# Performance work log

Measured on AMD Instinct MI355X. Metric: run time of the kernel, lower is better.

## Reference

```python
import jax, jax.numpy as jnp
import numpy as np
from jax import lax

B, CIN, H, W = 32, 256, 28, 28
COUT, KS, KEXP = 256, 3, 4
HIDDEN = int(CIN * 0.25)  # ratio hard-coded to 0.25 in the module


def setup_inputs() -> dict:
    key = jax.random.key(0)
    k1, k2, k3, k4 = jax.random.split(key, 4)
    x = jax.random.normal(k1, (B, CIN, H, W), dtype=jnp.float32)
    # SE (InvertedEx) params: fc1 (1x1 conv, no bias), fc2 (1x1 conv, bias)
    fc1_w = jax.random.normal(k2, (HIDDEN, CIN), dtype=jnp.float32) * np.float32(np.sqrt(2.0 / CIN))
    fc2_w = jax.random.normal(k3, (KEXP * COUT, HIDDEN), dtype=jnp.float32) * np.float32(np.sqrt(2.0 / HIDDEN))
    fc2_b = jnp.zeros((KEXP * COUT,), dtype=jnp.float32)
    # K expert conv kernels, he_std = sqrt(2) * (CIN*KS^2)^-0.5
    he_std = np.float32(np.sqrt(2.0) * (CIN * KS * KS) ** -0.5)
    weight = jax.random.normal(k4, (KEXP, COUT, CIN, KS, KS), dtype=jnp.float32) * he_std
    return {"x": x, "fc1_w": fc1_w, "fc2_w": fc2_w, "fc2_b": fc2_b, "weight": weight}


def reference(x, fc1_w, fc2_w, fc2_b, weight):
    # --- SE routing ---
    pooled = jnp.mean(x, axis=(2, 3))                        # [B, CIN]
    h = jax.nn.relu(pooled @ fc1_w.T)                        # [B, HIDDEN]
    y = (h @ fc2_w.T + fc2_b).reshape(B, KEXP, COUT)         # [B, K, COUT]
    prob = jax.nn.softmax(y / jnp.sqrt(jnp.float32(HIDDEN)), axis=1)  # softmax over K
    # --- aggregate per-sample kernels ---
    agg_w = jnp.einsum('bko,koihw->boihw', prob, weight)     # [B, COUT, CIN, KS, KS]
    # --- per-sample conv (batched implicit GEMM via vmap) ---
    def conv1(xi, wi):
        return lax.conv_general_dilated(
            xi[None], wi, window_strides=(1, 1), padding=((1, 1), (1, 1)),
            dimension_numbers=('NCHW', 'OIHW', 'NCHW'))[0]
    out = jax.vmap(conv1)(x, agg_w)                          # [B, COUT, H, W]
    return out
```

## Files before the change

### kernel.cpp

```cpp
#include <hip/hip_runtime.h>
#include <math.h>

#define B_    32
#define CIN_  256
#define HW_   784
#define H_    28
#define W_    28
#define COUT_ 256
#define KEXP_ 4
#define HID_  64

typedef short short8 __attribute__((ext_vector_type(8)));
typedef unsigned short ushort4v __attribute__((ext_vector_type(4)));
typedef float floatx16 __attribute__((ext_vector_type(16)));

__device__ __forceinline__ unsigned short f2bf(float f) {
    union { float f; unsigned int u; } v; v.f = f;
    unsigned int r = (v.u + 0x7FFFu + ((v.u >> 16) & 1u)) >> 16;
    return (unsigned short)r;
}

__global__ __launch_bounds__(256) void xpose_pool_kernel(const float* __restrict__ x,
                                                         unsigned short* __restrict__ x_t,
                                                         float* __restrict__ partial) {
    __shared__ float tile[32][33];
    int bid = blockIdx.x;
    int b   = bid / 200;
    int rem = bid - b * 200;
    int icg = rem / 25;
    int pxt = rem % 25;
    int ic0 = icg * 32;
    int px0 = pxt * 32;
    int t = threadIdx.x;
    int c = t & 31, rr = t >> 5;
    #pragma unroll
    for (int r = 0; r < 4; ++r) {
        int icr = rr + r * 8;
        int px = px0 + c;
        float v = (px < HW_) ? x[((size_t)(b * CIN_ + ic0 + icr)) * HW_ + px] : 0.f;
        tile[icr][c] = v;
    }
    __syncthreads();
    #pragma unroll
    for (int r = 0; r < 4; ++r) {
        int pxr = rr + r * 8;
        int px = px0 + pxr;
        if (px < HW_)
            x_t[((size_t)b * HW_ + px) * CIN_ + ic0 + c] = f2bf(tile[c][pxr]);
    }
    if (t < 32) {
        float s = 0.f;
        #pragma unroll
        for (int cc = 0; cc < 32; ++cc) s += tile[t][cc];
        partial[((size_t)b * 25 + pxt) * CIN_ + ic0 + t] = s * (1.0f / HW_);
    }
}

__global__ __launch_bounds__(256) void pool_kernel(const float* __restrict__ x,
                                                   float* __restrict__ pooled) {
    int w = blockIdx.x * 4 + (threadIdx.x >> 6);
    int lane = threadIdx.x & 63;
    const float* p = x + (size_t)w * HW_;
    float s = 0.f;
    for (int i = lane; i < HW_; i += 64) s += p[i];
    for (int off = 32; off; off >>= 1) s += __shfl_down(s, off);
    if (lane == 0) pooled[w] = s * (1.0f / HW_);
}

__global__ __launch_bounds__(256) void se3_kernel(const float* __restrict__ partial,
                                                  const float* __restrict__ fc1_w,
                                                  const float* __restrict__ fc2_w,
                                                  const float* __restrict__ fc2_b,
                                                  float* __restrict__ prob) {
    __shared__ float pl[CIN_];
    __shared__ float h[HID_];
    __shared__ float wb[16640];
    int b = blockIdx.x, t = threadIdx.x;
    {
        float s = 0.f;
        for (int pt = 0; pt < 25; ++pt)
            s += partial[((size_t)b * 25 + pt) * CIN_ + t];
        pl[t] = s;
    }
    #pragma unroll
    for (int i = 0; i < 16; ++i) {
        int l = t + i * 256;
        float4 v = *(const float4*)(fc1_w + (size_t)l * 4);
        int r = l >> 6, cc = (l & 63) * 4;
        float* dst = &wb[r * 257 + cc];
        dst[0] = v.x; dst[1] = v.y; dst[2] = v.z; dst[3] = v.w;
    }
    __syncthreads();
    if (t < HID_) {
        float s = 0.f;
        const float* wr = &wb[t * 257];
        for (int c = 0; c < CIN_; ++c) s += pl[c] * wr[c];
        h[t] = fmaxf(s, 0.f);
    }
    float yk[KEXP_];
    for (int k = 0; k < KEXP_; ++k) {
        __syncthreads();
        #pragma unroll
        for (int i = 0; i < 16; ++i) {
            int l = t + i * 256;
            float4 v = *(const float4*)(fc2_w + (size_t)k * COUT_ * HID_ + (size_t)l * 4);
            int o = l >> 4, jj = (l & 15) * 4;
            float* dst = &wb[o * 65 + jj];
            dst[0] = v.x; dst[1] = v.y; dst[2] = v.z; dst[3] = v.w;
        }
        __syncthreads();
        float s = fc2_b[k * COUT_ + t];
        const float* wr = &wb[t * 65];
        #pragma unroll
        for (int j = 0; j < HID_; ++j) s += h[j] * wr[j];
        yk[k] = s * 0.125f;
    }
    float m = yk[0];
    for (int k = 1; k < KEXP_; ++k) m = fmaxf(m, yk[k]);
    float e[KEXP_], sum = 0.f;
    for (int k = 0; k < KEXP_; ++k) { e[k] = expf(yk[k] - m); sum += e[k]; }
    float inv = 1.0f / sum;
    for (int k = 0; k < KEXP_; ++k)
        prob[b * (KEXP_ * COUT_) + k * COUT_ + t] = e[k] * inv;
}

__global__ __launch_bounds__(256) void se2_kernel(const float* __restrict__ pooled,
                                                  const float* __restrict__ fc1_w,
                                                  const float* __restrict__ fc2_w,
                                                  const float* __restrict__ fc2_b,
                                                  float* __restrict__ prob) {
    __shared__ float pl[CIN_];
    __shared__ float h[HID_];
    __shared__ float wb[16640];
    int b = blockIdx.x, t = threadIdx.x;
    pl[t] = pooled[b * CIN_ + t];
    #pragma unroll
    for (int i = 0; i < 16; ++i) {
        int l = t + i * 256;
        float4 v = *(const float4*)(fc1_w + (size_t)l * 4);
        int r = l >> 6, cc = (l & 63) * 4;
        float* dst = &wb[r * 257 + cc];
        dst[0] = v.x; dst[1] = v.y; dst[2] = v.z; dst[3] = v.w;
    }
    __syncthreads();
    if (t < HID_) {
        float s = 0.f;
        const float* wr = &wb[t * 257];
        for (int c = 0; c < CIN_; ++c) s += pl[c] * wr[c];
        h[t] = fmaxf(s, 0.f);
    }
    float yk[KEXP_];
    for (int k = 0; k < KEXP_; ++k) {
        __syncthreads();
        #pragma unroll
        for (int i = 0; i < 16; ++i) {
            int l = t + i * 256;
            float4 v = *(const float4*)(fc2_w + (size_t)k * COUT_ * HID_ + (size_t)l * 4);
            int o = l >> 4, jj = (l & 15) * 4;
            float* dst = &wb[o * 65 + jj];
            dst[0] = v.x; dst[1] = v.y; dst[2] = v.z; dst[3] = v.w;
        }
        __syncthreads();
        float s = fc2_b[k * COUT_ + t];
        const float* wr = &wb[t * 65];
        #pragma unroll
        for (int j = 0; j < HID_; ++j) s += h[j] * wr[j];
        yk[k] = s * 0.125f;
    }
    float m = yk[0];
    for (int k = 1; k < KEXP_; ++k) m = fmaxf(m, yk[k]);
    float e[KEXP_], sum = 0.f;
    for (int k = 0; k < KEXP_; ++k) { e[k] = expf(yk[k] - m); sum += e[k]; }
    float inv = 1.0f / sum;
    for (int k = 0; k < KEXP_; ++k)
        prob[b * (KEXP_ * COUT_) + k * COUT_ + t] = e[k] * inv;
}

__global__ __launch_bounds__(256) void agg3_kernel(const float* __restrict__ weight,
                                                   const float* __restrict__ prob,
                                                   unsigned short* __restrict__ agg) {
    __shared__ float ws_w[KEXP_ * CIN_ * 9];
    __shared__ float pb[KEXP_][8];
    int bid = blockIdx.x;
    int oc = bid & 255;
    int b0 = (bid >> 8) * 8;
    int t = threadIdx.x;
    #pragma unroll
    for (int i = 0; i < 9; ++i) {
        int e4 = t + i * 256;
        int k = e4 / 576;
        int r4 = e4 - k * 576;
        float4 v = *(const float4*)(weight + (size_t)k * 589824 + (size_t)oc * 2304 + (size_t)r4 * 4);
        *(float4*)&ws_w[e4 * 4] = v;
    }
    if (t < KEXP_ * 8) {
        int k = t >> 3, bb = t & 7;
        pb[k][bb] = prob[(size_t)(b0 + bb) * (KEXP_ * COUT_) + k * COUT_ + oc];
    }
    __syncthreads();
    int icg = t & 63, blane = t >> 6;
    for (int rs = 0; rs < 9; ++rs) {
        float wv[4][4];
        #pragma unroll
        for (int q = 0; q < 4; ++q)
            #pragma unroll
            for (int k = 0; k < 4; ++k)
                wv[q][k] = ws_w[k * 2304 + (icg * 4 + q) * 9 + rs];
        #pragma unroll
        for (int bb = 0; bb < 2; ++bb) {
            int bidx = blane * 2 + bb;
            float p0 = pb[0][bidx], p1 = pb[1][bidx], p2 = pb[2][bidx], p3 = pb[3][bidx];
            ushort4v pack;
            #pragma unroll
            for (int q = 0; q < 4; ++q) {
                float s = p0 * wv[q][0] + p1 * wv[q][1] + p2 * wv[q][2] + p3 * wv[q][3];
                pack[q] = f2bf(s);
            }
            *(ushort4v*)(agg + ((((size_t)(b0 + bidx) * 9 + rs) * COUT_ + oc)) * CIN_ + icg * 4) = pack;
        }
    }
}

__global__ __launch_bounds__(256, 1) void conv_mfma3_kernel(const unsigned short* __restrict__ x_t,
                                                            const unsigned short* __restrict__ agg,
                                                            float* __restrict__ out) {
    __shared__ __align__(16) short Xs[2][9 * 35 * 72];

    int gid = blockIdx.x;
    int b      = gid & 31;
    int oc0    = ((gid >> 5) & 1) * 128;
    int rowblk = gid >> 6;
    int py0 = rowblk * 7;

    int t = threadIdx.x;
    int lane = t & 63, w = t >> 6;
    int ml = lane & 31, kh = lane >> 5;

    floatx16 acc[7];
    #pragma unroll
    for (int j = 0; j < 7; ++j)
        #pragma unroll
        for (int r = 0; r < 16; ++r) acc[j][r] = 0.f;

    const unsigned short* xtb = x_t + (size_t)b * HW_ * CIN_;
    const unsigned short* aln = agg + (((size_t)b * 9 * COUT_) + oc0 + w * 32 + ml) * CIN_ + kh * 8;

    {
        #pragma unroll
        for (int i = 0; i < 10; ++i) {
            int l = t + i * 256;
            if (l < 2520) {
                int pos = l >> 3, g = l & 7;
                int row = pos / 35, col = pos - row * 35;
                int gy = py0 - 1 + row, gx = col - 1;
                short8 v = (short8)0;
                if ((unsigned)gy < 28u && (unsigned)gx < 28u)
                    v = *(const short8*)(xtb + ((size_t)(gy * W_ + gx)) * CIN_ + g * 8);
                *(short8*)&Xs[0][pos * 72 + g * 8] = v;
            }
        }
    }

    short8 Acur0, Acur1, Acur2, Anext0, Anext1, Anext2;
    Acur0 = *(const short8*)(aln + (size_t)(0 * 3 + 0) * (COUT_ * CIN_));
    Acur1 = *(const short8*)(aln + (size_t)(1 * 3 + 0) * (COUT_ * CIN_));
    Acur2 = *(const short8*)(aln + (size_t)(2 * 3 + 0) * (COUT_ * CIN_));
    int dxn = 1, kkn = 0, icn = 0;

    __syncthreads();

    for (int c = 0; c < 4; ++c) {
        int ic0 = c * 64;
        const short* xb = &Xs[c & 1][0];

        short8 Xl[10];
        if (c < 3) {
            #pragma unroll
            for (int i = 0; i < 10; ++i) {
                int l = t + i * 256;
                short8 v = (short8)0;
                if (l < 2520) {
                    int pos = l >> 3, g = l & 7;
                    int row = pos / 35, col = pos - row * 35;
                    int gy = py0 - 1 + row, gx = col - 1;
                    if ((unsigned)gy < 28u && (unsigned)gx < 28u)
                        v = *(const short8*)(xtb + ((size_t)(gy * W_ + gx)) * CIN_ + ic0 + 64 + g * 8);
                }
                Xl[i] = v;
            }
        }

        for (int kk = 0; kk < 4; ++kk) {
            for (int dx = 0; dx < 3; ++dx) {
                if (icn < 256) {
                    const unsigned short* ap = aln + icn + kkn * 16;
                    Anext0 = *(const short8*)(ap + (size_t)(0 * 3 + dxn) * (COUT_ * CIN_));
                    Anext1 = *(const short8*)(ap + (size_t)(1 * 3 + dxn) * (COUT_ * CIN_));
                    Anext2 = *(const short8*)(ap + (size_t)(2 * 3 + dxn) * (COUT_ * CIN_));
                    ++dxn;
                    if (dxn == 3) { dxn = 0; ++kkn; if (kkn == 4) { kkn = 0; icn += 64; } }
                }
                int va = (ml + dx) * 72 + kk * 16 + kh * 8;
                #pragma unroll
                for (int r = 0; r < 9; ++r) {
                    short8 Bf = *(const short8*)&xb[r * 2520 + va];
                    if (r <= 6)
                        acc[r]     = __builtin_amdgcn_mfma_f32_32x32x16_bf16(Acur0, Bf, acc[r], 0, 0, 0);
                    if (r >= 1 && r - 1 <= 6)
                        acc[r - 1] = __builtin_amdgcn_mfma_f32_32x32x16_bf16(Acur1, Bf, acc[r - 1], 0, 0, 0);
                    if (r >= 2)
                        acc[r - 2] = __builtin_amdgcn_mfma_f32_32x32x16_bf16(Acur2, Bf, acc[r - 2], 0, 0, 0);
                }
                Acur0 = Anext0; Acur1 = Anext1; Acur2 = Anext2;
            }
        }

        if (c < 3) {
            short* dstb = &Xs[(c & 1) ^ 1][0];
            #pragma unroll
            for (int i = 0; i < 10; ++i) {
                int l = t + i * 256;
                if (l < 2520) {
                    int pos = l >> 3, g = l & 7;
                    *(short8*)&dstb[pos * 72 + g * 8] = Xl[i];
                }
            }
        }
        __syncthreads();
    }

    if (ml < W_) {
        #pragma unroll
        for (int j = 0; j < 7; ++j) {
            float* op = out + ((size_t)(b * COUT_ + oc0 + w * 32)) * HW_ + (py0 + j) * W_ + ml;
            #pragma unroll
            for (int r = 0; r < 16; ++r) {
                int ocd = (r & 3) + 8 * (r >> 2) + 4 * kh;
                op[(size_t)ocd * HW_] = acc[j][r];
            }
        }
    }
}

__global__ __launch_bounds__(256) void conv_kernel(const float* __restrict__ x,
                                                   const float* __restrict__ weight,
                                                   const float* __restrict__ prob,
                                                   float* __restrict__ out) {
    __shared__ float xs[30 * 30];
    __shared__ float wagg[8][32][12];
    __shared__ float pl[KEXP_][8];

    int b  = blockIdx.x >> 5;
    int o0 = (blockIdx.x & 31) * 8;
    int t  = threadIdx.x;

    if (t < 32) {
        int k = t >> 3, oc = t & 7;
        pl[k][oc] = prob[b * (KEXP_ * COUT_) + k * COUT_ + o0 + oc];
    }
    int p0 = t;
    int pr[4], pc[4];
    bool pv[4];
    #pragma unroll
    for (int j = 0; j < 4; ++j) {
        int p = p0 + j * 256;
        pv[j] = p < HW_;
        pr[j] = p / W_;
        pc[j] = p % W_;
    }
    float acc[8][4];
    #pragma unroll
    for (int oc = 0; oc < 8; ++oc)
        #pragma unroll
        for (int j = 0; j < 4; ++j) acc[oc][j] = 0.f;

    int aoc = t >> 5, aii = t & 31;

    for (int ic0 = 0; ic0 < CIN_; ic0 += 32) {
        __syncthreads();
        {
            float w9[9];
            #pragma unroll
            for (int j = 0; j < 9; ++j) w9[j] = 0.f;
            int i = ic0 + aii;
            #pragma unroll
            for (int k = 0; k < KEXP_; ++k) {
                float pk = pl[k][aoc];
                const float* wp = weight + ((size_t)(k * COUT_ + o0 + aoc) * CIN_ + i) * 9;
                #pragma unroll
                for (int j = 0; j < 9; ++j) w9[j] += pk * wp[j];
            }
            #pragma unroll
            for (int j = 0; j < 9; ++j) wagg[aoc][aii][j] = w9[j];
        }
        for (int ii = 0; ii < 32; ++ii) {
            int i = ic0 + ii;
            __syncthreads();
            const float* xp = x + (size_t)(b * CIN_ + i) * HW_;
            for (int e = t; e < 900; e += 256) {
                int ry = e / 30, cx = e - ry * 30;
                int gy = ry - 1, gx = cx - 1;
                float v = 0.f;
                if ((unsigned)gy < 28u && (unsigned)gx < 28u) v = xp[gy * W_ + gx];
                xs[e] = v;
            }
            __syncthreads();
            float xv[4][9];
            #pragma unroll
            for (int j = 0; j < 4; ++j) {
                if (pv[j]) {
                    const float* xr = &xs[pr[j] * 30 + pc[j]];
                    xv[j][0] = xr[0];  xv[j][1] = xr[1];  xv[j][2] = xr[2];
                    xv[j][3] = xr[30]; xv[j][4] = xr[31]; xv[j][5] = xr[32];
                    xv[j][6] = xr[60]; xv[j][7] = xr[61]; xv[j][8] = xr[62];
                } else {
                    #pragma unroll
                    for (int q = 0; q < 9; ++q) xv[j][q] = 0.f;
                }
            }
            #pragma unroll
            for (int oc = 0; oc < 8; ++oc) {
                float4 wa = *(const float4*)&wagg[oc][ii][0];
                float4 wb2 = *(const float4*)&wagg[oc][ii][4];
                float  wc = wagg[oc][ii][8];
                #pragma unroll
                for (int j = 0; j < 4; ++j) {
                    acc[oc][j] += xv[j][0] * wa.x + xv[j][1] * wa.y + xv[j][2] * wa.z
                                + xv[j][3] * wa.w + xv[j][4] * wb2.x + xv[j][5] * wb2.y
                                + xv[j][6] * wb2.z + xv[j][7] * wb2.w + xv[j][8] * wc;
                }
            }
        }
    }
    #pragma unroll
    for (int oc = 0; oc < 8; ++oc) {
        float* op = out + (size_t)(b * COUT_ + o0 + oc) * HW_ + p0;
        #pragma unroll
        for (int j = 0; j < 4; ++j)
            if (pv[j]) op[j * 256] = acc[oc][j];
    }
}

extern "C" void kernel_launch(void* const* d_in, const int* in_sizes, int n_in,
                              void* d_out, int out_size, void* d_ws, size_t ws_size,
                              hipStream_t stream) {
    const float* x     = (const float*)d_in[0];
    const float* fc1_w = (const float*)d_in[1];
    const float* fc2_w = (const float*)d_in[2];
    const float* fc2_b = (const float*)d_in[3];
    const float* weight= (const float*)d_in[4];
    float* out = (float*)d_out;

    char* ws = (char*)d_ws;
    float* prob = (float*)(ws);
    unsigned short* x_t = (unsigned short*)(ws + 131072);
    unsigned short* agg = (unsigned short*)(ws + 12976128);
    float* partial = (float*)(ws + 12976128);
    const size_t WS_NEED = 12976128 + (size_t)B_ * 9 * COUT_ * CIN_ * 2;

    if (ws_size >= WS_NEED) {
        xpose_pool_kernel<<<B_ * 8 * 25, 256, 0, stream>>>(x, x_t, partial);
        se3_kernel<<<B_, 256, 0, stream>>>(partial, fc1_w, fc2_w, fc2_b, prob);
        agg3_kernel<<<4 * COUT_, 256, 0, stream>>>(weight, prob, agg);
        conv_mfma3_kernel<<<256, 256, 0, stream>>>(x_t, agg, out);
    } else {
        float* pooled = (float*)(ws + 131072);
        pool_kernel<<<(B_ * CIN_) / 4, 256, 0, stream>>>(x, pooled);
        se2_kernel<<<B_, 256, 0, stream>>>(pooled, fc1_w, fc2_w, fc2_b, prob);
        conv_kernel<<<B_ * (COUT_ / 8), 256, 0, stream>>>(x, weight, prob, out);
    }
}
```

Baseline: 149.9 us.

## Fuse SE routing into aggregation and store aggregated weights in MFMA-fragment layout

Merges the SE routing kernel into the weight-aggregation kernel, so each block recomputes the pooled vector, the hidden layer and the softmax for its 32 output channels and one sample. This removes a kernel launch and the round trip of the probability tensor. The aggregated bf16 weights are now written in a pre-swizzled layout where each lane's 8-element A fragment is contiguous, so the conv kernel's A loads coalesce instead of striding across CIN rows. The cost is that the SE work is repeated for every output-channel group, and the aggregation kernel reads expert weights straight from global memory with strided scalar loads instead of staging them in shared memory.

```diff
diff --git a/kernel.cpp b/kernel.cpp
--- a/kernel.cpp
+++ b/kernel.cpp
@@ -11,7 +11,6 @@
 #define HID_  64
 
 typedef short short8 __attribute__((ext_vector_type(8)));
-typedef unsigned short ushort4v __attribute__((ext_vector_type(4)));
 typedef float floatx16 __attribute__((ext_vector_type(16)));
 
 __device__ __forceinline__ unsigned short f2bf(float f) {
@@ -56,6 +55,200 @@
     }
 }
 
+__global__ __launch_bounds__(256) void agg6_kernel(const float* __restrict__ weight,
+                                                   const float* __restrict__ partial,
+                                                   const float* __restrict__ fc1_w,
+                                                   const float* __restrict__ fc2_w,
+                                                   const float* __restrict__ fc2_b,
+                                                   unsigned short* __restrict__ agg) {
+    __shared__ float pl[CIN_];
+    __shared__ float h[HID_];
+    __shared__ float pb[KEXP_][32];
+    int bid = blockIdx.x;
+    int b = bid & 31, ocg = bid >> 5;
+    int t = threadIdx.x;
+
+    {
+        float s = 0.f;
+        for (int pt = 0; pt < 25; ++pt)
+            s += partial[((size_t)b * 25 + pt) * CIN_ + t];
+        pl[t] = s;
+    }
+    __syncthreads();
+    {
+        int hi = t >> 2, q = t & 3;
+        const float* wr = fc1_w + (size_t)hi * CIN_ + q * 64;
+        const float* pr = &pl[q * 64];
+        float a = 0.f;
+        #pragma unroll
+        for (int j = 0; j < 64; ++j) a += pr[j] * wr[j];
+        a += __shfl_xor(a, 1);
+        a += __shfl_xor(a, 2);
+        if (q == 0) h[hi] = fmaxf(a, 0.f);
+    }
+    __syncthreads();
+    if (t < 128) {
+        int ol = t >> 2, k = t & 3;
+        int oc = ocg * 32 + ol;
+        const float* fr = fc2_w + ((size_t)(k * COUT_ + oc)) * HID_;
+        float y = fc2_b[k * COUT_ + oc];
+        #pragma unroll
+        for (int j = 0; j < HID_; ++j) y += h[j] * fr[j];
+        y *= 0.125f;
+        float m = fmaxf(y, __shfl_xor(y, 1));
+        m = fmaxf(m, __shfl_xor(m, 2));
+        float e = expf(y - m);
+        float s1 = e + __shfl_xor(e, 1);
+        float s2 = s1 + __shfl_xor(s1, 2);
+        pb[k][ol] = e / s2;
+    }
+    __syncthreads();
+
+    int oc_l = t & 31, gg = t >> 5;
+    int oc = ocg * 32 + oc_l;
+    float p0 = pb[0][oc_l], p1 = pb[1][oc_l], p2 = pb[2][oc_l], p3 = pb[3][oc_l];
+    const float* w0 = weight + (size_t)0 * 589824 + (size_t)oc * 2304;
+    const float* w1 = weight + (size_t)1 * 589824 + (size_t)oc * 2304;
+    const float* w2 = weight + (size_t)2 * 589824 + (size_t)oc * 2304;
+    const float* w3 = weight + (size_t)3 * 589824 + (size_t)oc * 2304;
+    #pragma unroll
+    for (int p = 0; p < 4; ++p) {
+        int g = p * 8 + gg;
+        int ic0 = g * 8;
+        for (int rs = 0; rs < 9; ++rs) {
+            unsigned short vals[8];
+            #pragma unroll
+            for (int j = 0; j < 8; ++j) {
+                int wi = (ic0 + j) * 9 + rs;
+                float s = p0 * w0[wi] + p1 * w1[wi] + p2 * w2[wi] + p3 * w3[wi];
+                vals[j] = f2bf(s);
+            }
+            size_t region = ((size_t)(b * 9 + rs) * 16 + (g >> 1)) * 8 + ocg;
+            *(short8*)(agg + region * 512 + ((g & 1) * 32 + oc_l) * 8) = *(short8*)vals;
+        }
+    }
+}
+
+__global__ __launch_bounds__(256, 1) void conv_mfma6_kernel(const unsigned short* __restrict__ x_t,
+                                                            const unsigned short* __restrict__ agg,
+                                                            float* __restrict__ out) {
+    __shared__ __align__(16) short Xs[2][9 * 35 * 72];
+
+    int gid = blockIdx.x;
+    int b      = gid & 31;
+    int half   = (gid >> 5) & 1;
+    int rowblk = gid >> 6;
+    int py0 = rowblk * 7;
+
+    int t = threadIdx.x;
+    int lane = t & 63, w = t >> 6;
+    int ml = lane & 31, kh = lane >> 5;
+    int oc0 = half * 128 + w * 32;
+    int ocg_w = half * 4 + w;
+
+    floatx16 acc[7];
+    #pragma unroll
+    for (int j = 0; j < 7; ++j)
+        #pragma unroll
+        for (int r = 0; r < 16; ++r) acc[j][r] = 0.f;
+
+    const unsigned short* xtb = x_t + (size_t)b * HW_ * CIN_;
+    const unsigned short* aln = agg + ((size_t)(b * 9 * 16 * 8 + ocg_w)) * 512 + lane * 8;
+
+    #pragma unroll
+    for (int i = 0; i < 10; ++i) {
+        int l = t + i * 256;
+        if (l < 2520) {
+            int pos = l >> 3, g = l & 7;
+            int row = pos / 35, col = pos - row * 35;
+            int gy = py0 - 1 + row, gx = col - 1;
+            short8 v = (short8)0;
+            if ((unsigned)gy < 28u && (unsigned)gx < 28u)
+                v = *(const short8*)(xtb + ((size_t)(gy * W_ + gx)) * CIN_ + g * 8);
+            *(short8*)&Xs[0][pos * 72 + g * 8] = v;
+        }
+    }
+
+    short8 Acur0, Acur1, Acur2, Anext0, Anext1, Anext2;
+    Acur0 = *(const short8*)(aln + (size_t)0 * 65536);
+    Acur1 = *(const short8*)(aln + (size_t)3 * 65536);
+    Acur2 = *(const short8*)(aln + (size_t)6 * 65536);
+    int dxn = 1, kkn = 0, icn = 0;
+
+    __syncthreads();
+
+    for (int c = 0; c < 4; ++c) {
+        const short* xb = &Xs[c & 1][0];
+
+        short8 Xl[10];
+        if (c < 3) {
+            #pragma unroll
+            for (int i = 0; i < 10; ++i) {
+                int l = t + i * 256;
+                short8 v = (short8)0;
+                if (l < 2520) {
+                    int pos = l >> 3, g = l & 7;
+                    int row = pos / 35, col = pos - row * 35;
+                    int gy = py0 - 1 + row, gx = col - 1;
+                    if ((unsigned)gy < 28u && (unsigned)gx < 28u)
+                        v = *(const short8*)(xtb + ((size_t)(gy * W_ + gx)) * CIN_ + c * 64 + 64 + g * 8);
+                }
+                Xl[i] = v;
+            }
+        }
+
+        for (int kk = 0; kk < 4; ++kk) {
+            for (int dx = 0; dx < 3; ++dx) {
+                if (icn < 256) {
+                    size_t iko = (size_t)((icn >> 4) + kkn) * 4096;
+                    Anext0 = *(const short8*)(aln + (size_t)(0 + dxn) * 65536 + iko);
+                    Anext1 = *(const short8*)(aln + (size_t)(3 + dxn) * 65536 + iko);
+                    Anext2 = *(const short8*)(aln + (size_t)(6 + dxn) * 65536 + iko);
+                    ++dxn;
+                    if (dxn == 3) { dxn = 0; ++kkn; if (kkn == 4) { kkn = 0; icn += 64; } }
+                }
+                int va = (ml + dx) * 72 + kk * 16 + kh * 8;
+                #pragma unroll
+                for (int r = 0; r < 9; ++r) {
+                    short8 Bf = *(const short8*)&xb[r * 2520 + va];
+                    if (r <= 6)
+                        acc[r]     = __builtin_amdgcn_mfma_f32_32x32x16_bf16(Acur0, Bf, acc[r], 0, 0, 0);
+                    if (r >= 1 && r - 1 <= 6)
+                        acc[r - 1] = __builtin_amdgcn_mfma_f32_32x32x16_bf16(Acur1, Bf, acc[r - 1], 0, 0, 0);
+                    if (r >= 2)
+                        acc[r - 2] = __builtin_amdgcn_mfma_f32_32x32x16_bf16(Acur2, Bf, acc[r - 2], 0, 0, 0);
+                }
+                Acur0 = Anext0; Acur1 = Anext1; Acur2 = Anext2;
+            }
+        }
+
+        if (c < 3) {
+            short* dstb = &Xs[(c & 1) ^ 1][0];
+            #pragma unroll
+            for (int i = 0; i < 10; ++i) {
+                int l = t + i * 256;
+                if (l < 2520) {
+                    int pos = l >> 3, g = l & 7;
+                    *(short8*)&dstb[pos * 72 + g * 8] = Xl[i];
+                }
+            }
+        }
+        __syncthreads();
+    }
+
+    if (ml < W_) {
+        #pragma unroll
+        for (int j = 0; j < 7; ++j) {
+            float* op = out + ((size_t)(b * COUT_ + oc0)) * HW_ + (py0 + j) * W_ + ml;
+            #pragma unroll
+            for (int r = 0; r < 16; ++r) {
+                int ocd = (r & 3) + 8 * (r >> 2) + 4 * kh;
+                op[(size_t)ocd * HW_] = acc[j][r];
+            }
+        }
+    }
+}
+
 __global__ __launch_bounds__(256) void pool_kernel(const float* __restrict__ x,
                                                    float* __restrict__ pooled) {
     int w = blockIdx.x * 4 + (threadIdx.x >> 6);
@@ -65,63 +258,6 @@
     for (int i = lane; i < HW_; i += 64) s += p[i];
     for (int off = 32; off; off >>= 1) s += __shfl_down(s, off);
     if (lane == 0) pooled[w] = s * (1.0f / HW_);
-}
-
-__global__ __launch_bounds__(256) void se3_kernel(const float* __restrict__ partial,
-                                                  const float* __restrict__ fc1_w,
-                                                  const float* __restrict__ fc2_w,
-                                                  const float* __restrict__ fc2_b,
-                                                  float* __restrict__ prob) {
-    __shared__ float pl[CIN_];
-    __shared__ float h[HID_];
-    __shared__ float wb[16640];
-    int b = blockIdx.x, t = threadIdx.x;
-    {
-        float s = 0.f;
-        for (int pt = 0; pt < 25; ++pt)
-            s += partial[((size_t)b * 25 + pt) * CIN_ + t];
-        pl[t] = s;
-    }
-    #pragma unroll
-    for (int i = 0; i < 16; ++i) {
-        int l = t + i * 256;
-        float4 v = *(const float4*)(fc1_w + (size_t)l * 4);
-        int r = l >> 6, cc = (l & 63) * 4;
-        float* dst = &wb[r * 257 + cc];
-        dst[0] = v.x; dst[1] = v.y; dst[2] = v.z; dst[3] = v.w;
-    }
-    __syncthreads();
-    if (t < HID_) {
-        float s = 0.f;
-        const float* wr = &wb[t * 257];
-        for (int c = 0; c < CIN_; ++c) s += pl[c] * wr[c];
-        h[t] = fmaxf(s, 0.f);
-    }
-    float yk[KEXP_];
-    for (int k = 0; k < KEXP_; ++k) {
-        __syncthreads();
-        #pragma unroll
-        for (int i = 0; i < 16; ++i) {
-            int l = t + i * 256;
-            float4 v = *(const float4*)(fc2_w + (size_t)k * COUT_ * HID_ + (size_t)l * 4);
-            int o = l >> 4, jj = (l & 15) * 4;
-            float* dst = &wb[o * 65 + jj];
-            dst[0] = v.x; dst[1] = v.y; dst[2] = v.z; dst[3] = v.w;
-        }
-        __syncthreads();
-        float s = fc2_b[k * COUT_ + t];
-        const float* wr = &wb[t * 65];
-        #pragma unroll
-        for (int j = 0; j < HID_; ++j) s += h[j] * wr[j];
-        yk[k] = s * 0.125f;
-    }
-    float m = yk[0];
-    for (int k = 1; k < KEXP_; ++k) m = fmaxf(m, yk[k]);
-    float e[KEXP_], sum = 0.f;
-    for (int k = 0; k < KEXP_; ++k) { e[k] = expf(yk[k] - m); sum += e[k]; }
-    float inv = 1.0f / sum;
-    for (int k = 0; k < KEXP_; ++k)
-        prob[b * (KEXP_ * COUT_) + k * COUT_ + t] = e[k] * inv;
 }
 
 __global__ __launch_bounds__(256) void se2_kernel(const float* __restrict__ pooled,
@@ -176,172 +312,6 @@
         prob[b * (KEXP_ * COUT_) + k * COUT_ + t] = e[k] * inv;
 }
 
-__global__ __launch_bounds__(256) void agg3_kernel(const float* __restrict__ weight,
-                                                   const float* __restrict__ prob,
-                                                   unsigned short* __restrict__ agg) {
-    __shared__ float ws_w[KEXP_ * CIN_ * 9];
-    __shared__ float pb[KEXP_][8];
-    int bid = blockIdx.x;
-    int oc = bid & 255;
-    int b0 = (bid >> 8) * 8;
-    int t = threadIdx.x;
-    #pragma unroll
-    for (int i = 0; i < 9; ++i) {
-        int e4 = t + i * 256;
-        int k = e4 / 576;
-        int r4 = e4 - k * 576;
-        float4 v = *(const float4*)(weight + (size_t)k * 589824 + (size_t)oc * 2304 + (size_t)r4 * 4);
-        *(float4*)&ws_w[e4 * 4] = v;
-    }
-    if (t < KEXP_ * 8) {
-        int k = t >> 3, bb = t & 7;
-        pb[k][bb] = prob[(size_t)(b0 + bb) * (KEXP_ * COUT_) + k * COUT_ + oc];
-    }
-    __syncthreads();
-    int icg = t & 63, blane = t >> 6;
-    for (int rs = 0; rs < 9; ++rs) {
-        float wv[4][4];
-        #pragma unroll
-        for (int q = 0; q < 4; ++q)
-            #pragma unroll
-            for (int k = 0; k < 4; ++k)
-                wv[q][k] = ws_w[k * 2304 + (icg * 4 + q) * 9 + rs];
-        #pragma unroll
-        for (int bb = 0; bb < 2; ++bb) {
-            int bidx = blane * 2 + bb;
-            float p0 = pb[0][bidx], p1 = pb[1][bidx], p2 = pb[2][bidx], p3 = pb[3][bidx];
-            ushort4v pack;
-            #pragma unroll
-            for (int q = 0; q < 4; ++q) {
-                float s = p0 * wv[q][0] + p1 * wv[q][1] + p2 * wv[q][2] + p3 * wv[q][3];
-                pack[q] = f2bf(s);
-            }
-            *(ushort4v*)(agg + ((((size_t)(b0 + bidx) * 9 + rs) * COUT_ + oc)) * CIN_ + icg * 4) = pack;
-        }
-    }
-}
-
-__global__ __launch_bounds__(256, 1) void conv_mfma3_kernel(const unsigned short* __restrict__ x_t,
-                                                            const unsigned short* __restrict__ agg,
-                                                            float* __restrict__ out) {
-    __shared__ __align__(16) short Xs[2][9 * 35 * 72];
-
-    int gid = blockIdx.x;
-    int b      = gid & 31;
-    int oc0    = ((gid >> 5) & 1) * 128;
-    int rowblk = gid >> 6;
-    int py0 = rowblk * 7;
-
-    int t = threadIdx.x;
-    int lane = t & 63, w = t >> 6;
-    int ml = lane & 31, kh = lane >> 5;
-
-    floatx16 acc[7];
-    #pragma unroll
-    for (int j = 0; j < 7; ++j)
-        #pragma unroll
-        for (int r = 0; r < 16; ++r) acc[j][r] = 0.f;
-
-    const unsigned short* xtb = x_t + (size_t)b * HW_ * CIN_;
-    const unsigned short* aln = agg + (((size_t)b * 9 * COUT_) + oc0 + w * 32 + ml) * CIN_ + kh * 8;
-
-    {
-        #pragma unroll
-        for (int i = 0; i < 10; ++i) {
-            int l = t + i * 256;
-            if (l < 2520) {
-                int pos = l >> 3, g = l & 7;
-                int row = pos / 35, col = pos - row * 35;
-                int gy = py0 - 1 + row, gx = col - 1;
-                short8 v = (short8)0;
-                if ((unsigned)gy < 28u && (unsigned)gx < 28u)
-                    v = *(const short8*)(xtb + ((size_t)(gy * W_ + gx)) * CIN_ + g * 8);
-                *(short8*)&Xs[0][pos * 72 + g * 8] = v;
-            }
-        }
-    }
-
-    short8 Acur0, Acur1, Acur2, Anext0, Anext1, Anext2;
-    Acur0 = *(const short8*)(aln + (size_t)(0 * 3 + 0) * (COUT_ * CIN_));
-    Acur1 = *(const short8*)(aln + (size_t)(1 * 3 + 0) * (COUT_ * CIN_));
-    Acur2 = *(const short8*)(aln + (size_t)(2 * 3 + 0) * (COUT_ * CIN_));
-    int dxn = 1, kkn = 0, icn = 0;
-
-    __syncthreads();
-
-    for (int c = 0; c < 4; ++c) {
-        int ic0 = c * 64;
-        const short* xb = &Xs[c & 1][0];
-
-        short8 Xl[10];
-        if (c < 3) {
-            #pragma unroll
-            for (int i = 0; i < 10; ++i) {
-                int l = t + i * 256;
-                short8 v = (short8)0;
-                if (l < 2520) {
-                    int pos = l >> 3, g = l & 7;
-                    int row = pos / 35, col = pos - row * 35;
-                    int gy = py0 - 1 + row, gx = col - 1;
-                    if ((unsigned)gy < 28u && (unsigned)gx < 28u)
-                        v = *(const short8*)(xtb + ((size_t)(gy * W_ + gx)) * CIN_ + ic0 + 64 + g * 8);
-                }
-                Xl[i] = v;
-            }
-        }
-
-        for (int kk = 0; kk < 4; ++kk) {
-            for (int dx = 0; dx < 3; ++dx) {
-                if (icn < 256) {
-                    const unsigned short* ap = aln + icn + kkn * 16;
-                    Anext0 = *(const short8*)(ap + (size_t)(0 * 3 + dxn) * (COUT_ * CIN_));
-                    Anext1 = *(const short8*)(ap + (size_t)(1 * 3 + dxn) * (COUT_ * CIN_));
-                    Anext2 = *(const short8*)(ap + (size_t)(2 * 3 + dxn) * (COUT_ * CIN_));
-                    ++dxn;
-                    if (dxn == 3) { dxn = 0; ++kkn; if (kkn == 4) { kkn = 0; icn += 64; } }
-                }
-                int va = (ml + dx) * 72 + kk * 16 + kh * 8;
-                #pragma unroll
-                for (int r = 0; r < 9; ++r) {
-                    short8 Bf = *(const short8*)&xb[r * 2520 + va];
-                    if (r <= 6)
-                        acc[r]     = __builtin_amdgcn_mfma_f32_32x32x16_bf16(Acur0, Bf, acc[r], 0, 0, 0);
-                    if (r >= 1 && r - 1 <= 6)
-                        acc[r - 1] = __builtin_amdgcn_mfma_f32_32x32x16_bf16(Acur1, Bf, acc[r - 1], 0, 0, 0);
-                    if (r >= 2)
-                        acc[r - 2] = __builtin_amdgcn_mfma_f32_32x32x16_bf16(Acur2, Bf, acc[r - 2], 0, 0, 0);
-                }
-                Acur0 = Anext0; Acur1 = Anext1; Acur2 = Anext2;
-            }
-        }
-
-        if (c < 3) {
-            short* dstb = &Xs[(c & 1) ^ 1][0];
-            #pragma unroll
-            for (int i = 0; i < 10; ++i) {
-                int l = t + i * 256;
-                if (l < 2520) {
-                    int pos = l >> 3, g = l & 7;
-                    *(short8*)&dstb[pos * 72 + g * 8] = Xl[i];
-                }
-            }
-        }
-        __syncthreads();
-    }
-
-    if (ml < W_) {
-        #pragma unroll
-        for (int j = 0; j < 7; ++j) {
-            float* op = out + ((size_t)(b * COUT_ + oc0 + w * 32)) * HW_ + (py0 + j) * W_ + ml;
-            #pragma unroll
-            for (int r = 0; r < 16; ++r) {
-                int ocd = (r & 3) + 8 * (r >> 2) + 4 * kh;
-                op[(size_t)ocd * HW_] = acc[j][r];
-            }
-        }
-    }
-}
-
 __global__ __launch_bounds__(256) void conv_kernel(const float* __restrict__ x,
                                                    const float* __restrict__ weight,
                                                    const float* __restrict__ prob,
@@ -452,18 +422,17 @@
     float* out = (float*)d_out;
 
     char* ws = (char*)d_ws;
-    float* prob = (float*)(ws);
-    unsigned short* x_t = (unsigned short*)(ws + 131072);
-    unsigned short* agg = (unsigned short*)(ws + 12976128);
-    float* partial = (float*)(ws + 12976128);
-    const size_t WS_NEED = 12976128 + (size_t)B_ * 9 * COUT_ * CIN_ * 2;
+    float* partial = (float*)(ws);
+    unsigned short* x_t = (unsigned short*)(ws + 851968);
+    unsigned short* agg = (unsigned short*)(ws + 13697024);
+    const size_t WS_NEED = 13697024 + 37748736;
 
     if (ws_size >= WS_NEED) {
         xpose_pool_kernel<<<B_ * 8 * 25, 256, 0, stream>>>(x, x_t, partial);
-        se3_kernel<<<B_, 256, 0, stream>>>(partial, fc1_w, fc2_w, fc2_b, prob);
-        agg3_kernel<<<4 * COUT_, 256, 0, stream>>>(weight, prob, agg);
-        conv_mfma3_kernel<<<256, 256, 0, stream>>>(x_t, agg, out);
+        agg6_kernel<<<256, 256, 0, stream>>>(weight, partial, fc1_w, fc2_w, fc2_b, agg);
+        conv_mfma6_kernel<<<256, 256, 0, stream>>>(x_t, agg, out);
     } else {
+        float* prob = (float*)(ws);
         float* pooled = (float*)(ws + 131072);
         pool_kernel<<<(B_ * CIN_) / 4, 256, 0, stream>>>(x, pooled);
         se2_kernel<<<B_, 256, 0, stream>>>(pooled, fc1_w, fc2_w, fc2_b, prob);
```

After: 262.4 us. +75.1%, slower.
